# Kernel tuning notes

Hardware: AMD Instinct MI355X
Metric: run time of the kernel (lower is better)

The kernel has to match this reference:

```python
import jax, jax.numpy as jnp
import numpy as np

PAA_SIZE = 64  # init_kwargs paa_size
GAF_TYPE = 'GADF'  # init_kwargs GAF_type


def setup_inputs() -> dict:
    key = jax.random.key(0)
    x = jax.random.uniform(key, (256, 4096, 32), dtype=jnp.float32)
    return {"x": x}


def reference(x):
    # x: [B, T, C]
    B, T, C = x.shape
    # --- rescale: per-sample, per-channel min-max over time axis -> [0, 1]
    x_min = jnp.min(x, axis=1, keepdims=True)
    x_max = jnp.max(x, axis=1, keepdims=True)
    r = (x - x_min) / (x_max - x_min)            # [B, T, C]
    # --- PAA: strided mean over bins of length size = T // paa_size
    size = T // PAA_SIZE
    p = r[:, : PAA_SIZE * size].reshape(B, PAA_SIZE, size, C).sum(axis=2) / size  # [B, P, C]
    # --- GAF construction
    y = jnp.sqrt(1.0 - p * p)                    # [B, P, C]
    if GAF_TYPE == 'GASF':
        # out[b,i,j,c] = x_i x_j - y_i y_j (symmetric)
        out = jnp.einsum('bic,bjc->bijc', p, p) - jnp.einsum('bic,bjc->bijc', y, y)
    else:  # 'GADF'
        # original: -transpose(y x^T - x y^T) => out[b,i,j,c] = y_i x_j - x_i y_j
        out = jnp.einsum('bic,bjc->bijc', y, p) - jnp.einsum('bic,bjc->bijc', p, y)
    return out  # [B, paa_size, paa_size, C]
```

## Files before the change

### kernel.cpp

```cpp
#include <hip/hip_runtime.h>
#include <math.h>


#define BB   256
#define TT   4096
#define CC   32
#define PP   64
#define PSTR 33

typedef float f32x4 __attribute__((ext_vector_type(4)));

#define SEG_FLOATS  (BB * PP * CC)
#define MM_FLOATS   (BB * 32 * CC)
#define WS_FLOATS   (SEG_FLOATS + 2 * MM_FLOATS)
#define WS_BYTES    (WS_FLOATS * 4)

__device__ __forceinline__ float4 f4min(float4 a, float4 b) {
    return make_float4(fminf(a.x,b.x), fminf(a.y,b.y), fminf(a.z,b.z), fminf(a.w,b.w));
}
__device__ __forceinline__ float4 f4max(float4 a, float4 b) {
    return make_float4(fmaxf(a.x,b.x), fmaxf(a.y,b.y), fmaxf(a.z,b.z), fmaxf(a.w,b.w));
}
__device__ __forceinline__ void f4add(float4& a, float4 v) {
    a.x += v.x; a.y += v.y; a.z += v.z; a.w += v.w;
}
__device__ __forceinline__ float4 shflxor4(float4 v, int m) {
    return make_float4(__shfl_xor(v.x, m), __shfl_xor(v.y, m),
                       __shfl_xor(v.z, m), __shfl_xor(v.w, m));
}
__device__ __forceinline__ void ntstore4(float4* dst, float4 v) {
    f32x4 t; t.x = v.x; t.y = v.y; t.z = v.z; t.w = v.w;
    __builtin_nontemporal_store(t, (f32x4*)dst);
}

__global__ __launch_bounds__(256, 8) void gaf_stats(const float* __restrict__ x,
                                                    float* __restrict__ ws) {
    const int tid  = threadIdx.x;
    const int lane = tid & 63;
    const int wave = tid >> 6;
    const int cg   = lane & 7;
    const int blk  = blockIdx.x;
    const int b    = blk >> 3;
    const int ch   = blk & 7;

    const float4* base = (const float4*)x + (size_t)b * (TT * CC / 4)
                         + ch * 4096 + wave * 1024 + lane;

    const float FBIG = 3.402823466e+38f;
    float4 mn = make_float4(FBIG, FBIG, FBIG, FBIG);
    float4 mx = make_float4(-FBIG, -FBIG, -FBIG, -FBIG);
    float4 acc0 = make_float4(0.f, 0.f, 0.f, 0.f);
    float4 acc1 = make_float4(0.f, 0.f, 0.f, 0.f);

    float4 buf[8];
    #pragma unroll
    for (int u = 0; u < 8; ++u) buf[u] = base[u * 64];
    #pragma unroll
    for (int u = 0; u < 8; ++u) { mn = f4min(mn, buf[u]); mx = f4max(mx, buf[u]); f4add(acc0, buf[u]); }
    #pragma unroll
    for (int u = 0; u < 8; ++u) buf[u] = base[(8 + u) * 64];
    #pragma unroll
    for (int u = 0; u < 8; ++u) { mn = f4min(mn, buf[u]); mx = f4max(mx, buf[u]); f4add(acc1, buf[u]); }

    #pragma unroll
    for (int m = 8; m <= 32; m <<= 1) {
        mn = f4min(mn, shflxor4(mn, m));
        mx = f4max(mx, shflxor4(mx, m));
        f4add(acc0, shflxor4(acc0, m));
        f4add(acc1, shflxor4(acc1, m));
    }

    if (lane < 8) {
        const int s0 = ch * 8 + wave * 2;
        *(float4*)&ws[(size_t)b * (PP * CC) + s0 * CC + cg * 4]       = acc0;
        *(float4*)&ws[(size_t)b * (PP * CC) + (s0 + 1) * CC + cg * 4] = acc1;
        const int k = ch * 4 + wave;
        *(float4*)&ws[SEG_FLOATS             + (size_t)b * (32 * CC) + k * CC + cg * 4] = mn;
        *(float4*)&ws[SEG_FLOATS + MM_FLOATS + (size_t)b * (32 * CC) + k * CC + cg * 4] = mx;
    }
}

__global__ __launch_bounds__(256, 4) void gaf_outer(const float* __restrict__ ws,
                                                    float* __restrict__ out) {
    __shared__ float sp[PP * PSTR];
    __shared__ float sy[PP * PSTR];
    __shared__ float4 lmn[32];
    __shared__ float4 lmx[32];

    const int tid  = threadIdx.x;
    const int lane = tid & 63;
    const int wave = tid >> 6;
    const int cg   = lane & 7;
    const int blk  = blockIdx.x;
    const int b    = blk >> 2;
    const int i0   = (blk & 3) * 16;

    {
        const int k = wave * 8 + (lane >> 3);
        float4 mnk = *(const float4*)&ws[SEG_FLOATS             + (size_t)b * (32 * CC) + k * CC + cg * 4];
        float4 mxk = *(const float4*)&ws[SEG_FLOATS + MM_FLOATS + (size_t)b * (32 * CC) + k * CC + cg * 4];
        #pragma unroll
        for (int m = 8; m <= 32; m <<= 1) {
            mnk = f4min(mnk, shflxor4(mnk, m));
            mxk = f4max(mxk, shflxor4(mxk, m));
        }
        if (lane < 8) { lmn[wave * 8 + cg] = mnk; lmx[wave * 8 + cg] = mxk; }
    }
    __syncthreads();

    {
        const int cq = tid & 7;
        float4 mnf = f4min(f4min(lmn[cq], lmn[8 + cq]), f4min(lmn[16 + cq], lmn[24 + cq]));
        float4 mxf = f4max(f4max(lmx[cq], lmx[8 + cq]), f4max(lmx[16 + cq], lmx[24 + cq]));
        float4 inv;
        inv.x = 1.0f / (mxf.x - mnf.x);  inv.y = 1.0f / (mxf.y - mnf.y);
        inv.z = 1.0f / (mxf.z - mnf.z);  inv.w = 1.0f / (mxf.w - mnf.w);
        const float s64 = 1.0f / 64.0f;
        #pragma unroll
        for (int h = 0; h < 2; ++h) {
            const int s = (tid >> 3) + h * 32;
            float4 sum = *(const float4*)&ws[(size_t)b * (PP * CC) + s * CC + cq * 4];
            float4 p, y;
            p.x = (sum.x * s64 - mnf.x) * inv.x;  p.y = (sum.y * s64 - mnf.y) * inv.y;
            p.z = (sum.z * s64 - mnf.z) * inv.z;  p.w = (sum.w * s64 - mnf.w) * inv.w;
            y.x = sqrtf(fmaxf(1.f - p.x * p.x, 0.f));  y.y = sqrtf(fmaxf(1.f - p.y * p.y, 0.f));
            y.z = sqrtf(fmaxf(1.f - p.z * p.z, 0.f));  y.w = sqrtf(fmaxf(1.f - p.w * p.w, 0.f));
            *(float4*)&sp[s * PSTR + cq * 4] = p;
            *(float4*)&sy[s * PSTR + cq * 4] = y;
        }
    }
    __syncthreads();

    const int jrow = lane >> 3;
    float4 pj[8], yj[8];
    #pragma unroll
    for (int jc = 0; jc < 8; ++jc) {
        const int j = jc * 8 + jrow;
        pj[jc] = *(const float4*)&sp[j * PSTR + cg * 4];
        yj[jc] = *(const float4*)&sy[j * PSTR + cg * 4];
    }

    float4* ob = (float4*)out + (size_t)b * (PP * PP * CC / 4) + lane;

    #pragma unroll
    for (int ii = 0; ii < 4; ++ii) {
        const int i = i0 + wave * 4 + ii;
        const float4 pi = *(const float4*)&sp[i * PSTR + cg * 4];
        const float4 yi = *(const float4*)&sy[i * PSTR + cg * 4];
        #pragma unroll
        for (int jc = 0; jc < 8; ++jc) {
            float4 r;
            r.x = yi.x * pj[jc].x - pi.x * yj[jc].x;
            r.y = yi.y * pj[jc].y - pi.y * yj[jc].y;
            r.z = yi.z * pj[jc].z - pi.z * yj[jc].z;
            r.w = yi.w * pj[jc].w - pi.w * yj[jc].w;
            ntstore4(&ob[i * 512 + jc * 64], r);
        }
    }
}

__global__ __launch_bounds__(1024, 4) void gaf_fused(const float* __restrict__ x,
                                                     float* __restrict__ out) {
    __shared__ float sp[PP * PSTR];
    __shared__ float sy[PP * PSTR];
    __shared__ float redmin[16 * CC];
    __shared__ float redmax[16 * CC];

    const int tid  = threadIdx.x;
    const int lane = tid & 63;
    const int wave = tid >> 6;
    const int cg   = lane & 7;
    const int b    = blockIdx.x;

    const float4* xw = (const float4*)x + (size_t)b * (TT * CC / 4) + wave * 2048 + lane;

    const float FBIG = 3.402823466e+38f;
    float4 mn = make_float4(FBIG, FBIG, FBIG, FBIG);
    float4 mx = make_float4(-FBIG, -FBIG, -FBIG, -FBIG);
    float4 acc[4];
    #pragma unroll
    for (int g = 0; g < 4; ++g) acc[g] = make_float4(0.f, 0.f, 0.f, 0.f);

    #pragma unroll
    for (int g = 0; g < 4; ++g) {
        float4 buf[8];
        #pragma unroll
        for (int u = 0; u < 8; ++u) buf[u] = xw[(g * 8 + u) * 64];
        #pragma unroll
        for (int u = 0; u < 8; ++u) {
            mn = f4min(mn, buf[u]); mx = f4max(mx, buf[u]); f4add(acc[g], buf[u]);
        }
    }

    #pragma unroll
    for (int m = 8; m <= 32; m <<= 1) {
        mn = f4min(mn, shflxor4(mn, m));
        mx = f4max(mx, shflxor4(mx, m));
        #pragma unroll
        for (int g = 0; g < 4; ++g) f4add(acc[g], shflxor4(acc[g], m));
    }

    if (lane < 8) {
        *(float4*)&redmin[wave * CC + cg * 4] = mn;
        *(float4*)&redmax[wave * CC + cg * 4] = mx;
    }
    __syncthreads();

    float4 gmn = *(const float4*)&redmin[0 * CC + cg * 4];
    float4 gmx = *(const float4*)&redmax[0 * CC + cg * 4];
    #pragma unroll
    for (int w = 1; w < 16; ++w) {
        gmn = f4min(gmn, *(const float4*)&redmin[w * CC + cg * 4]);
        gmx = f4max(gmx, *(const float4*)&redmax[w * CC + cg * 4]);
    }

    float4 inv;
    inv.x = 1.0f / (gmx.x - gmn.x);  inv.y = 1.0f / (gmx.y - gmn.y);
    inv.z = 1.0f / (gmx.z - gmn.z);  inv.w = 1.0f / (gmx.w - gmn.w);
    const float s64 = 1.0f / 64.0f;

    if (lane < 8) {
        #pragma unroll
        for (int g = 0; g < 4; ++g) {
            float4 p, y;
            p.x = (acc[g].x * s64 - gmn.x) * inv.x;  p.y = (acc[g].y * s64 - gmn.y) * inv.y;
            p.z = (acc[g].z * s64 - gmn.z) * inv.z;  p.w = (acc[g].w * s64 - gmn.w) * inv.w;
            y.x = sqrtf(fmaxf(1.f - p.x * p.x, 0.f));  y.y = sqrtf(fmaxf(1.f - p.y * p.y, 0.f));
            y.z = sqrtf(fmaxf(1.f - p.z * p.z, 0.f));  y.w = sqrtf(fmaxf(1.f - p.w * p.w, 0.f));
            const int s = wave * 4 + g;
            *(float4*)&sp[s * PSTR + cg * 4] = p;
            *(float4*)&sy[s * PSTR + cg * 4] = y;
        }
    }
    __syncthreads();

    const int jrow = lane >> 3;
    float4 pj[8], yj[8];
    #pragma unroll
    for (int jc = 0; jc < 8; ++jc) {
        const int j = jc * 8 + jrow;
        pj[jc] = *(const float4*)&sp[j * PSTR + cg * 4];
        yj[jc] = *(const float4*)&sy[j * PSTR + cg * 4];
    }

    float4* ob = (float4*)out + (size_t)b * (PP * PP * CC / 4) + wave * 2048 + lane;

    #pragma unroll
    for (int ii = 0; ii < 4; ++ii) {
        const float4 pi = *(const float4*)&sp[(wave * 4 + ii) * PSTR + cg * 4];
        const float4 yi = *(const float4*)&sy[(wave * 4 + ii) * PSTR + cg * 4];
        #pragma unroll
        for (int jc = 0; jc < 8; ++jc) {
            float4 r;
            r.x = yi.x * pj[jc].x - pi.x * yj[jc].x;
            r.y = yi.y * pj[jc].y - pi.y * yj[jc].y;
            r.z = yi.z * pj[jc].z - pi.z * yj[jc].z;
            r.w = yi.w * pj[jc].w - pi.w * yj[jc].w;
            ob[ii * 512 + jc * 64] = r;
        }
    }
}

extern "C" void kernel_launch(void* const* d_in, const int* in_sizes, int n_in,
                              void* d_out, int out_size, void* d_ws, size_t ws_size,
                              hipStream_t stream) {
    const float* x = (const float*)d_in[0];
    float* out = (float*)d_out;
    if (d_ws != nullptr && ws_size >= (size_t)WS_BYTES) {
        float* ws = (float*)d_ws;
        gaf_stats<<<BB * 8, 256, 0, stream>>>(x, ws);
        gaf_outer<<<BB * 4, 256, 0, stream>>>(ws, out);
    } else {
        gaf_fused<<<BB, 1024, 0, stream>>>(x, out);
    }
}
```

Before: 231.5 us.

## Remap stats kernel so each wave reduces one segment across four batches

The stats kernel now assigns each wave a single PAA segment and loops over four batches spaced 64 apart, so consecutive waves read contiguous 8KB chunks. It pre-reduces min/max across the four waves in shared memory, which shrinks the min/max workspace from 32 to 16 partials per batch, and launches a fixed 1024 blocks. The outer kernel is adjusted to read the new layout, and its nontemporal stores are replaced with plain stores. The aim is better memory access locality and less workspace traffic. The cost is extra shared-memory synchronisation, and dropping the nontemporal hint may pollute the cache.

```diff
diff --git a/kernel.cpp b/kernel.cpp
--- a/kernel.cpp
+++ b/kernel.cpp
@@ -8,12 +8,13 @@
 #define PP   64
 #define PSTR 33
 
-typedef float f32x4 __attribute__((ext_vector_type(4)));
-
-#define SEG_FLOATS  (BB * PP * CC)
-#define MM_FLOATS   (BB * 32 * CC)
-#define WS_FLOATS   (SEG_FLOATS + 2 * MM_FLOATS)
-#define WS_BYTES    (WS_FLOATS * 4)
+#define SUM_OFF    0
+#define SUM_FLOATS (BB * PP * CC)
+#define MN_OFF     SUM_FLOATS
+#define MM_FLOATS  (BB * 16 * CC)
+#define MX_OFF     (MN_OFF + MM_FLOATS)
+#define WS_FLOATS  (MX_OFF + MM_FLOATS)
+#define WS_BYTES   (WS_FLOATS * 4)
 
 __device__ __forceinline__ float4 f4min(float4 a, float4 b) {
     return make_float4(fminf(a.x,b.x), fminf(a.y,b.y), fminf(a.z,b.z), fminf(a.w,b.w));
@@ -28,55 +29,69 @@
     return make_float4(__shfl_xor(v.x, m), __shfl_xor(v.y, m),
                        __shfl_xor(v.z, m), __shfl_xor(v.w, m));
 }
-__device__ __forceinline__ void ntstore4(float4* dst, float4 v) {
-    f32x4 t; t.x = v.x; t.y = v.y; t.z = v.z; t.w = v.w;
-    __builtin_nontemporal_store(t, (f32x4*)dst);
-}
-
-__global__ __launch_bounds__(256, 8) void gaf_stats(const float* __restrict__ x,
+
+__global__ __launch_bounds__(256, 4) void gaf_stats(const float* __restrict__ x,
                                                     float* __restrict__ ws) {
+    __shared__ float4 cmn[4][4][8];
+    __shared__ float4 cmx[4][4][8];
+
     const int tid  = threadIdx.x;
     const int lane = tid & 63;
     const int wave = tid >> 6;
     const int cg   = lane & 7;
     const int blk  = blockIdx.x;
-    const int b    = blk >> 3;
-    const int ch   = blk & 7;
-
-    const float4* base = (const float4*)x + (size_t)b * (TT * CC / 4)
-                         + ch * 4096 + wave * 1024 + lane;
-
-    const float FBIG = 3.402823466e+38f;
-    float4 mn = make_float4(FBIG, FBIG, FBIG, FBIG);
-    float4 mx = make_float4(-FBIG, -FBIG, -FBIG, -FBIG);
-    float4 acc0 = make_float4(0.f, 0.f, 0.f, 0.f);
-    float4 acc1 = make_float4(0.f, 0.f, 0.f, 0.f);
-
-    float4 buf[8];
-    #pragma unroll
-    for (int u = 0; u < 8; ++u) buf[u] = base[u * 64];
-    #pragma unroll
-    for (int u = 0; u < 8; ++u) { mn = f4min(mn, buf[u]); mx = f4max(mx, buf[u]); f4add(acc0, buf[u]); }
-    #pragma unroll
-    for (int u = 0; u < 8; ++u) buf[u] = base[(8 + u) * 64];
-    #pragma unroll
-    for (int u = 0; u < 8; ++u) { mn = f4min(mn, buf[u]); mx = f4max(mx, buf[u]); f4add(acc1, buf[u]); }
-
-    #pragma unroll
-    for (int m = 8; m <= 32; m <<= 1) {
-        mn = f4min(mn, shflxor4(mn, m));
-        mx = f4max(mx, shflxor4(mx, m));
-        f4add(acc0, shflxor4(acc0, m));
-        f4add(acc1, shflxor4(acc1, m));
+    const int W    = blk * 4 + wave;
+    const int s    = W & 63;
+    const int bofs = W >> 6;
+
+    const float4* xb = (const float4*)x + (size_t)W * 512 + lane;
+
+    float4 mnS[4], mxS[4];
+
+    #pragma unroll
+    for (int u = 0; u < 4; ++u) {
+        const float4* g = xb + (size_t)u * 2097152;
+        float4 buf[8];
+        #pragma unroll
+        for (int v = 0; v < 8; ++v) buf[v] = g[v * 64];
+
+        float4 mn = buf[0], mx = buf[0], acc = buf[0];
+        #pragma unroll
+        for (int v = 1; v < 8; ++v) {
+            mn = f4min(mn, buf[v]); mx = f4max(mx, buf[v]); f4add(acc, buf[v]);
+        }
+        #pragma unroll
+        for (int m = 8; m <= 32; m <<= 1) {
+            mn = f4min(mn, shflxor4(mn, m));
+            mx = f4max(mx, shflxor4(mx, m));
+            f4add(acc, shflxor4(acc, m));
+        }
+        mnS[u] = mn; mxS[u] = mx;
+
+        if (lane < 8) {
+            const int b = u * 64 + bofs;
+            *(float4*)&ws[SUM_OFF + b * (PP * CC) + s * CC + cg * 4] = acc;
+        }
     }
 
     if (lane < 8) {
-        const int s0 = ch * 8 + wave * 2;
-        *(float4*)&ws[(size_t)b * (PP * CC) + s0 * CC + cg * 4]       = acc0;
-        *(float4*)&ws[(size_t)b * (PP * CC) + (s0 + 1) * CC + cg * 4] = acc1;
-        const int k = ch * 4 + wave;
-        *(float4*)&ws[SEG_FLOATS             + (size_t)b * (32 * CC) + k * CC + cg * 4] = mn;
-        *(float4*)&ws[SEG_FLOATS + MM_FLOATS + (size_t)b * (32 * CC) + k * CC + cg * 4] = mx;
+        #pragma unroll
+        for (int u = 0; u < 4; ++u) { cmn[wave][u][cg] = mnS[u]; cmx[wave][u][cg] = mxS[u]; }
+    }
+    __syncthreads();
+
+    if (wave < 2 && lane < 32) {
+        const int u = lane >> 3, c = lane & 7;
+        const int b = u * 64 + bofs;
+        if (wave == 0) {
+            float4 m = f4min(f4min(cmn[0][u][c], cmn[1][u][c]),
+                             f4min(cmn[2][u][c], cmn[3][u][c]));
+            *(float4*)&ws[MN_OFF + b * (16 * CC) + (blk & 15) * CC + c * 4] = m;
+        } else {
+            float4 m = f4max(f4max(cmx[0][u][c], cmx[1][u][c]),
+                             f4max(cmx[2][u][c], cmx[3][u][c]));
+            *(float4*)&ws[MX_OFF + b * (16 * CC) + (blk & 15) * CC + c * 4] = m;
+        }
     }
 }
 
@@ -96,9 +111,9 @@
     const int i0   = (blk & 3) * 16;
 
     {
-        const int k = wave * 8 + (lane >> 3);
-        float4 mnk = *(const float4*)&ws[SEG_FLOATS             + (size_t)b * (32 * CC) + k * CC + cg * 4];
-        float4 mxk = *(const float4*)&ws[SEG_FLOATS + MM_FLOATS + (size_t)b * (32 * CC) + k * CC + cg * 4];
+        const int r = (wave & 1) * 8 + (lane >> 3);
+        float4 mnk = *(const float4*)&ws[MN_OFF + b * (16 * CC) + r * CC + cg * 4];
+        float4 mxk = *(const float4*)&ws[MX_OFF + b * (16 * CC) + r * CC + cg * 4];
         #pragma unroll
         for (int m = 8; m <= 32; m <<= 1) {
             mnk = f4min(mnk, shflxor4(mnk, m));
@@ -119,7 +134,7 @@
         #pragma unroll
         for (int h = 0; h < 2; ++h) {
             const int s = (tid >> 3) + h * 32;
-            float4 sum = *(const float4*)&ws[(size_t)b * (PP * CC) + s * CC + cq * 4];
+            float4 sum = *(const float4*)&ws[SUM_OFF + b * (PP * CC) + s * CC + cq * 4];
             float4 p, y;
             p.x = (sum.x * s64 - mnf.x) * inv.x;  p.y = (sum.y * s64 - mnf.y) * inv.y;
             p.z = (sum.z * s64 - mnf.z) * inv.z;  p.w = (sum.w * s64 - mnf.w) * inv.w;
@@ -154,7 +169,7 @@
             r.y = yi.y * pj[jc].y - pi.y * yj[jc].y;
             r.z = yi.z * pj[jc].z - pi.z * yj[jc].z;
             r.w = yi.w * pj[jc].w - pi.w * yj[jc].w;
-            ntstore4(&ob[i * 512 + jc * 64], r);
+            ob[i * 512 + jc * 64] = r;
         }
     }
 }
@@ -268,7 +283,7 @@
     float* out = (float*)d_out;
     if (d_ws != nullptr && ws_size >= (size_t)WS_BYTES) {
         float* ws = (float*)d_ws;
-        gaf_stats<<<BB * 8, 256, 0, stream>>>(x, ws);
+        gaf_stats<<<1024, 256, 0, stream>>>(x, ws);
         gaf_outer<<<BB * 4, 256, 0, stream>>>(ws, out);
     } else {
         gaf_fused<<<BB, 1024, 0, stream>>>(x, out);
```

Measured after the change: 236.3 us. 2.0% more time.
